# Kernel tuning notes

Hardware: AMD Instinct MI355X
Metric: run time of the kernel (lower is better)

Reference implementation:

```python
import jax, jax.numpy as jnp
import numpy as np

B, S, I, H, O = 64, 4096, 256, 256, 128


def setup_inputs() -> dict:
    key = jax.random.key(0)
    ks = jax.random.split(key, 7)
    s_in = 1.0 / np.sqrt(I)
    s_h = 1.0 / np.sqrt(H)
    return {
        "x": jax.random.normal(ks[0], (B, S, I), dtype=jnp.float32),
        "Wax_w": jax.random.uniform(ks[1], (H, I), jnp.float32, -s_in, s_in),
        "Wax_b": jax.random.uniform(ks[2], (H,), jnp.float32, -s_in, s_in),
        "Waa_w": jax.random.uniform(ks[3], (H, H), jnp.float32, -s_h, s_h),
        "Waa_b": jax.random.uniform(ks[4], (H,), jnp.float32, -s_h, s_h),
        "Wya_w": jax.random.uniform(ks[5], (O, H), jnp.float32, -s_h, s_h),
        "Wya_b": jax.random.uniform(ks[6], (O,), jnp.float32, -s_h, s_h),
    }


def reference(x, Wax_w, Wax_b, Waa_w, Waa_b, Wya_w, Wya_b):
    # Precompute input projections for all timesteps in one big GEMM: [B,S,H]
    xp = jnp.einsum("bsi,hi->bsh", x, Wax_w) + Wax_b

    def step(a_prev, xp_t):
        a_next = jnp.tanh(xp_t + a_prev @ Waa_w.T + Waa_b)
        return a_next, None

    a0 = jnp.zeros((x.shape[0], Waa_w.shape[0]), dtype=x.dtype)
    a_last, _ = jax.lax.scan(step, a0, jnp.swapaxes(xp, 0, 1))  # scan over S
    return jax.nn.sigmoid(a_last @ Wya_w.T + Wya_b)
```

## Files before the change

kernel.cpp:

```cpp
#include <hip/hip_runtime.h>
#include <hip/hip_fp16.h>


typedef _Float16 f16x8 __attribute__((ext_vector_type(8)));
typedef _Float16 f16x4 __attribute__((ext_vector_type(4)));
typedef _Float16 f16x2 __attribute__((ext_vector_type(2)));
typedef float    f32x4 __attribute__((ext_vector_type(4)));

#define FDOT2(a, b, c) __builtin_amdgcn_fdot2((a), (b), (c), false)

template <int D>
__device__ __forceinline__ float rorf(float v) {
    return __builtin_bit_cast(float,
        __builtin_amdgcn_update_dpp(0, __builtin_bit_cast(int, v),
                                    0x120 + D, 0xF, 0xF, true));
}

__global__ __launch_bounds__(512) void k_xp(
    const float* __restrict__ x, const float* __restrict__ Ww,
    const float* __restrict__ Wb, _Float16* __restrict__ xp,
    int c, int T_C, int logT)
{
    __shared__ __align__(16) _Float16 As[64 * 264];
    const int tid  = threadIdx.x;
    const int lane = tid & 63;
    const int wv   = tid >> 6;
    const int l15  = lane & 15;
    const int lk   = lane >> 4;
    const int n0   = wv * 32;

    f16x8 bfr[2][8];
#pragma unroll
    for (int nt = 0; nt < 2; ++nt) {
        const float* wrow = Ww + (size_t)(n0 + nt * 16 + l15) * 256;
#pragma unroll
        for (int kt = 0; kt < 8; ++kt) {
            const float4* wp = (const float4*)(wrow + kt * 32 + lk * 8);
            float4 v0 = wp[0], v1 = wp[1];
            f16x8 f;
            f[0] = (_Float16)v0.x; f[1] = (_Float16)v0.y;
            f[2] = (_Float16)v0.z; f[3] = (_Float16)v0.w;
            f[4] = (_Float16)v1.x; f[5] = (_Float16)v1.y;
            f[6] = (_Float16)v1.z; f[7] = (_Float16)v1.w;
            bfr[nt][kt] = f;
        }
    }
    const float bias0 = Wb[n0 + l15];
    const float bias1 = Wb[n0 + 16 + l15];

    {
        const int arow = tid >> 3;
        const int acol = (tid & 7) * 32;
        const int r    = blockIdx.x * 64 + arow;
        const int bb   = r >> logT;
        const int tl   = r & (T_C - 1);
        const float4* s4 = (const float4*)(x + ((size_t)(bb * 4096 + c * T_C + tl) << 8) + acol);
        _Float16* d = As + arow * 264 + acol;
#pragma unroll
        for (int q = 0; q < 4; ++q) {
            float4 v0 = s4[2 * q], v1 = s4[2 * q + 1];
            f16x8 p;
            p[0] = (_Float16)v0.x; p[1] = (_Float16)v0.y;
            p[2] = (_Float16)v0.z; p[3] = (_Float16)v0.w;
            p[4] = (_Float16)v1.x; p[5] = (_Float16)v1.y;
            p[6] = (_Float16)v1.z; p[7] = (_Float16)v1.w;
            *(f16x8*)(d + q * 8) = p;
        }
    }
    __syncthreads();

    f32x4 acc[4][2] = {};
#pragma unroll
    for (int kt = 0; kt < 8; ++kt) {
#pragma unroll
        for (int mt = 0; mt < 4; ++mt) {
            f16x8 af = *(const f16x8*)(As + (mt * 16 + l15) * 264 + kt * 32 + lk * 8);
            acc[mt][0] = __builtin_amdgcn_mfma_f32_16x16x32_f16(af, bfr[0][kt], acc[mt][0], 0, 0, 0);
            acc[mt][1] = __builtin_amdgcn_mfma_f32_16x16x32_f16(af, bfr[1][kt], acc[mt][1], 0, 0, 0);
        }
    }

    const int base = blockIdx.x * 64;
#pragma unroll
    for (int mt = 0; mt < 4; ++mt) {
        const int rr  = base + mt * 16 + lk * 4;
        const int bb2 = rr >> logT;
        const int tt  = rr & (T_C - 1);
#pragma unroll
        for (int nt = 0; nt < 2; ++nt) {
            const int   h    = n0 + nt * 16 + l15;
            const float bias = (nt == 0) ? bias0 : bias1;
            f16x4 pk;
#pragma unroll
            for (int r2 = 0; r2 < 4; ++r2) pk[r2] = (_Float16)(acc[mt][nt][r2] + bias);
            *(f16x4*)(xp + ((size_t)(bb2 * 256 + h)) * T_C + tt) = pk;
        }
    }
}

__global__ __launch_bounds__(1024) void k_rnn(
    const _Float16* __restrict__ xp, const float* __restrict__ Waa,
    const float* __restrict__ Wab, const float* __restrict__ Wya,
    const float* __restrict__ Wyb, float* __restrict__ out,
    unsigned short* __restrict__ a_state,
    int c, int T_C, int is_last)
{
    __shared__ __align__(16) _Float16 aL[2][16][24];
    __shared__ float afin[256];
    const int tid   = threadIdx.x;
    const int lane  = tid & 63;
    const int w     = tid >> 6;
    const int k     = lane & 15;
    const int g     = lane >> 4;
    const int rbase = w * 16 + g * 4;
    const int myrow = rbase + (k & 3);
    const int b     = blockIdx.x;
    const bool wlane = (k & 12) == 0;

    f16x2 wr[4][8];
#pragma unroll
    for (int i = 0; i < 4; ++i) {
        const float4* wp = (const float4*)(Waa + (size_t)(rbase + ((k + i) & 3)) * 256 + k * 16);
#pragma unroll
        for (int q = 0; q < 4; ++q) {
            float4 v = wp[q];
            f16x2 t0; t0[0] = (_Float16)v.x; t0[1] = (_Float16)v.y;
            f16x2 t1; t1[0] = (_Float16)v.z; t1[1] = (_Float16)v.w;
            wr[i][2 * q]     = t0;
            wr[i][2 * q + 1] = t1;
        }
    }
    const float bias = Wab[myrow];

    if (tid < 256) {
        unsigned short v = 0;
        if (c != 0) v = a_state[b * 256 + tid];
        aL[0][tid >> 4][tid & 15] = __builtin_bit_cast(_Float16, v);
    }
    __syncthreads();

    const _Float16* xph = xp + ((size_t)(b * 256 + myrow)) * T_C;
    f16x8 xq = *(const f16x8*)(xph);

    const _Float16* rp0 = &aL[0][k][0];
    const _Float16* rp1 = &aL[1][k][0];
    _Float16* wq0 = &aL[1][w][g * 4 + k];
    _Float16* wq1 = &aL[0][w][g * 4 + k];

#define RNN_STEP(J, FIN)                                                     \
    {                                                                        \
        const _Float16* rp = ((J) & 1) ? rp1 : rp0;                          \
        uint4 r0 = *(const uint4*)(rp);                                      \
        uint4 r1 = *(const uint4*)(rp + 8);                                  \
        float bx = bias + (float)xq[(J)];                                    \
        f16x2 a2[8];                                                         \
        a2[0] = __builtin_bit_cast(f16x2, r0.x);                             \
        a2[1] = __builtin_bit_cast(f16x2, r0.y);                             \
        a2[2] = __builtin_bit_cast(f16x2, r0.z);                             \
        a2[3] = __builtin_bit_cast(f16x2, r0.w);                             \
        a2[4] = __builtin_bit_cast(f16x2, r1.x);                             \
        a2[5] = __builtin_bit_cast(f16x2, r1.y);                             \
        a2[6] = __builtin_bit_cast(f16x2, r1.z);                             \
        a2[7] = __builtin_bit_cast(f16x2, r1.w);                             \
        float s0 = 0.f, s1 = 0.f, s2 = 0.f, s3 = 0.f;                        \
        _Pragma("unroll")                                                    \
        for (int q = 0; q < 8; ++q) {                                        \
            s0 = FDOT2(wr[0][q], a2[q], s0);                                 \
            s1 = FDOT2(wr[1][q], a2[q], s1);                                 \
            s2 = FDOT2(wr[2][q], a2[q], s2);                                 \
            s3 = FDOT2(wr[3][q], a2[q], s3);                                 \
        }                                                                    \
        float p0 = s0 + rorf<8>(s0);                                         \
        float p1 = s1 + rorf<8>(s1);                                         \
        float p2 = s2 + rorf<8>(s2);                                         \
        float p3 = s3 + rorf<8>(s3);                                         \
        float q0 = p0 + rorf<4>(p0);                                         \
        float q1 = p1 + rorf<4>(p1);                                         \
        float q2 = p2 + rorf<4>(p2);                                         \
        float q3 = p3 + rorf<4>(p3);                                         \
        float acc = (q0 + rorf<1>(q1)) + (rorf<2>(q2) + rorf<3>(q3));        \
        float z  = bx + acc;                                                 \
        float e2 = __expf(2.f * z);                                          \
        float a  = fmaf(-2.f, __builtin_amdgcn_rcpf(e2 + 1.f), 1.f);         \
        _Float16 ah = (_Float16)a;                                           \
        if (wlane) *(((J) & 1) ? wq1 : wq0) = ah;                            \
        if (FIN) {                                                           \
            afin[myrow] = a;                                                 \
            a_state[b * 256 + myrow] = __builtin_bit_cast(unsigned short, ah);\
        }                                                                    \
        asm volatile("s_waitcnt lgkmcnt(0)" ::: "memory");                   \
        __builtin_amdgcn_s_barrier();                                        \
        asm volatile("" ::: "memory");                                       \
    }

    for (int tb = 0; tb + 8 < T_C; tb += 8) {
        f16x8 xn = *(const f16x8*)(xph + tb + 8);
        RNN_STEP(0, false) RNN_STEP(1, false) RNN_STEP(2, false) RNN_STEP(3, false)
        RNN_STEP(4, false) RNN_STEP(5, false) RNN_STEP(6, false) RNN_STEP(7, false)
        xq = xn;
    }
    RNN_STEP(0, false) RNN_STEP(1, false) RNN_STEP(2, false) RNN_STEP(3, false)
    RNN_STEP(4, false) RNN_STEP(5, false) RNN_STEP(6, false) RNN_STEP(7, true)
#undef RNN_STEP

    if (is_last) {
        const int o  = tid >> 3;
        const int k8 = tid & 7;
        const float4* wp = (const float4*)(Wya + (size_t)o * 256 + k8 * 32);
        const float4* ap = (const float4*)(afin + k8 * 32);
        float s = 0.f;
#pragma unroll
        for (int i = 0; i < 8; ++i) {
            float4 wv4 = wp[i];
            float4 a4  = ap[i];
            s += wv4.x * a4.x + wv4.y * a4.y + wv4.z * a4.z + wv4.w * a4.w;
        }
        s += __shfl_xor(s, 1);
        s += __shfl_xor(s, 2);
        s += __shfl_xor(s, 4);
        if (k8 == 0)
            out[b * 128 + o] = __builtin_amdgcn_rcpf(1.f + __expf(-(s + Wyb[o])));
    }
}

extern "C" void kernel_launch(void* const* d_in, const int* in_sizes, int n_in,
                              void* d_out, int out_size, void* d_ws, size_t ws_size,
                              hipStream_t stream)
{
    (void)in_sizes; (void)n_in; (void)out_size;
    const float* x    = (const float*)d_in[0];
    const float* Waxw = (const float*)d_in[1];
    const float* Waxb = (const float*)d_in[2];
    const float* Waaw = (const float*)d_in[3];
    const float* Waab = (const float*)d_in[4];
    const float* Wyaw = (const float*)d_in[5];
    const float* Wyab = (const float*)d_in[6];
    float* out = (float*)d_out;

    int T_C = 4096, logT = 12;
    while (T_C > 32 && (size_t)64 * T_C * 256 * 2 + 32768 > ws_size) { T_C >>= 1; --logT; }

    _Float16* xp = (_Float16*)d_ws;
    unsigned short* a_state =
        (unsigned short*)((char*)d_ws + (size_t)64 * T_C * 256 * 2);

    const int nc = 4096 / T_C;
    for (int ci = 0; ci < nc; ++ci) {
        k_xp<<<dim3(T_C), dim3(512), 0, stream>>>(x, Waxw, Waxb, xp, ci, T_C, logT);
        k_rnn<<<dim3(64), dim3(1024), 0, stream>>>(xp, Waaw, Waab, Wyaw, Wyab,
                                                   out, a_state, ci, T_C, ci == nc - 1);
    }
}
```

Measured before the change: 2.271 ms.

## Batch 16 RNN chains per block and compute recurrence with MFMA

The recurrent kernel now processes 16 batch chains per block (4 blocks of 512 threads) and computes the hidden-state matvec as a 16x16x32 f16 MFMA GEMM, with the weights held in registers and the state double-buffered in LDS. This replaces 64 blocks doing per-chain fdot2 plus DPP reductions. The recurrent bias is folded into the input projection kernel, and xp loads are double-buffered across 4-step groups. The cost is that only 4 CUs do the serial recurrence, so each step's MFMA chain plus barrier latency sets the speed.

Measured after the change: 4.406 ms. 94.0% more time.

```diff
diff --git a/kernel.cpp b/kernel.cpp
--- a/kernel.cpp
+++ b/kernel.cpp
@@ -4,22 +4,12 @@
 
 typedef _Float16 f16x8 __attribute__((ext_vector_type(8)));
 typedef _Float16 f16x4 __attribute__((ext_vector_type(4)));
-typedef _Float16 f16x2 __attribute__((ext_vector_type(2)));
 typedef float    f32x4 __attribute__((ext_vector_type(4)));
-
-#define FDOT2(a, b, c) __builtin_amdgcn_fdot2((a), (b), (c), false)
-
-template <int D>
-__device__ __forceinline__ float rorf(float v) {
-    return __builtin_bit_cast(float,
-        __builtin_amdgcn_update_dpp(0, __builtin_bit_cast(int, v),
-                                    0x120 + D, 0xF, 0xF, true));
-}
 
 __global__ __launch_bounds__(512) void k_xp(
     const float* __restrict__ x, const float* __restrict__ Ww,
-    const float* __restrict__ Wb, _Float16* __restrict__ xp,
-    int c, int T_C, int logT)
+    const float* __restrict__ Wb, const float* __restrict__ Wab,
+    _Float16* __restrict__ xp, int c, int T_C, int logT)
 {
     __shared__ __align__(16) _Float16 As[64 * 264];
     const int tid  = threadIdx.x;
@@ -45,8 +35,8 @@
             bfr[nt][kt] = f;
         }
     }
-    const float bias0 = Wb[n0 + l15];
-    const float bias1 = Wb[n0 + 16 + l15];
+    const float bias0 = Wb[n0 + l15]      + Wab[n0 + l15];
+    const float bias1 = Wb[n0 + 16 + l15] + Wab[n0 + 16 + l15];
 
     {
         const int arow = tid >> 3;
@@ -98,128 +88,141 @@
     }
 }
 
-__global__ __launch_bounds__(1024) void k_rnn(
+__global__ __launch_bounds__(512)
+__attribute__((amdgpu_waves_per_eu(2, 2)))
+void k_rnn(
     const _Float16* __restrict__ xp, const float* __restrict__ Waa,
-    const float* __restrict__ Wab, const float* __restrict__ Wya,
-    const float* __restrict__ Wyb, float* __restrict__ out,
-    unsigned short* __restrict__ a_state,
+    const float* __restrict__ Wya, const float* __restrict__ Wyb,
+    float* __restrict__ out, unsigned short* __restrict__ a_state,
     int c, int T_C, int is_last)
 {
-    __shared__ __align__(16) _Float16 aL[2][16][24];
-    __shared__ float afin[256];
-    const int tid   = threadIdx.x;
-    const int lane  = tid & 63;
-    const int w     = tid >> 6;
-    const int k     = lane & 15;
-    const int g     = lane >> 4;
-    const int rbase = w * 16 + g * 4;
-    const int myrow = rbase + (k & 3);
-    const int b     = blockIdx.x;
-    const bool wlane = (k & 12) == 0;
-
-    f16x2 wr[4][8];
-#pragma unroll
-    for (int i = 0; i < 4; ++i) {
-        const float4* wp = (const float4*)(Waa + (size_t)(rbase + ((k + i) & 3)) * 256 + k * 16);
-#pragma unroll
-        for (int q = 0; q < 4; ++q) {
-            float4 v = wp[q];
-            f16x2 t0; t0[0] = (_Float16)v.x; t0[1] = (_Float16)v.y;
-            f16x2 t1; t1[0] = (_Float16)v.z; t1[1] = (_Float16)v.w;
-            wr[i][2 * q]     = t0;
-            wr[i][2 * q + 1] = t1;
-        }
-    }
-    const float bias = Wab[myrow];
-
-    if (tid < 256) {
-        unsigned short v = 0;
-        if (c != 0) v = a_state[b * 256 + tid];
-        aL[0][tid >> 4][tid & 15] = __builtin_bit_cast(_Float16, v);
+    __shared__ __align__(16) _Float16 aL[2][16][264];
+    const int tid  = threadIdx.x;
+    const int lane = tid & 63;
+    const int wv   = tid >> 6;
+    const int i15  = lane & 15;
+    const int g    = lane >> 4;
+    const int blk  = blockIdx.x;
+    const int chain_g = blk * 16 + i15;
+
+    f16x8 wa0[8], wa1[8];
+    {
+        const float* w0 = Waa + (size_t)(wv * 32 + i15) * 256 + g * 8;
+        const float* w1 = w0 + 16 * 256;
+#pragma unroll
+        for (int kk = 0; kk < 8; ++kk) {
+            const float4* p0 = (const float4*)(w0 + kk * 32);
+            float4 va = p0[0], vb = p0[1];
+            f16x8 f;
+            f[0] = (_Float16)va.x; f[1] = (_Float16)va.y;
+            f[2] = (_Float16)va.z; f[3] = (_Float16)va.w;
+            f[4] = (_Float16)vb.x; f[5] = (_Float16)vb.y;
+            f[6] = (_Float16)vb.z; f[7] = (_Float16)vb.w;
+            wa0[kk] = f;
+            const float4* p1 = (const float4*)(w1 + kk * 32);
+            float4 vc = p1[0], vd = p1[1];
+            f16x8 f2;
+            f2[0] = (_Float16)vc.x; f2[1] = (_Float16)vc.y;
+            f2[2] = (_Float16)vc.z; f2[3] = (_Float16)vc.w;
+            f2[4] = (_Float16)vd.x; f2[5] = (_Float16)vd.y;
+            f2[6] = (_Float16)vd.z; f2[7] = (_Float16)vd.w;
+            wa1[kk] = f2;
+        }
+    }
+
+    {
+        const int e = tid * 8, ch = e >> 8, k0 = e & 255;
+        if (c == 0) {
+            f16x8 z = {};
+            *(f16x8*)&aL[0][ch][k0] = z;
+        } else {
+            *(uint4*)&aL[0][ch][k0] =
+                *(const uint4*)&a_state[((size_t)(blk * 16 + ch) << 8) + k0];
+        }
     }
     __syncthreads();
 
-    const _Float16* xph = xp + ((size_t)(b * 256 + myrow)) * T_C;
-    f16x8 xq = *(const f16x8*)(xph);
-
-    const _Float16* rp0 = &aL[0][k][0];
-    const _Float16* rp1 = &aL[1][k][0];
-    _Float16* wq0 = &aL[1][w][g * 4 + k];
-    _Float16* wq1 = &aL[0][w][g * 4 + k];
-
-#define RNN_STEP(J, FIN)                                                     \
+    const _Float16* xpb =
+        xp + ((size_t)(chain_g * 256 + wv * 32 + g * 4)) * T_C;
+    f16x4 xqA[2][4], xqB[2][4];
+
+#define LOADX(X, T)                                                          \
     {                                                                        \
-        const _Float16* rp = ((J) & 1) ? rp1 : rp0;                          \
-        uint4 r0 = *(const uint4*)(rp);                                      \
-        uint4 r1 = *(const uint4*)(rp + 8);                                  \
-        float bx = bias + (float)xq[(J)];                                    \
-        f16x2 a2[8];                                                         \
-        a2[0] = __builtin_bit_cast(f16x2, r0.x);                             \
-        a2[1] = __builtin_bit_cast(f16x2, r0.y);                             \
-        a2[2] = __builtin_bit_cast(f16x2, r0.z);                             \
-        a2[3] = __builtin_bit_cast(f16x2, r0.w);                             \
-        a2[4] = __builtin_bit_cast(f16x2, r1.x);                             \
-        a2[5] = __builtin_bit_cast(f16x2, r1.y);                             \
-        a2[6] = __builtin_bit_cast(f16x2, r1.z);                             \
-        a2[7] = __builtin_bit_cast(f16x2, r1.w);                             \
-        float s0 = 0.f, s1 = 0.f, s2 = 0.f, s3 = 0.f;                        \
         _Pragma("unroll")                                                    \
-        for (int q = 0; q < 8; ++q) {                                        \
-            s0 = FDOT2(wr[0][q], a2[q], s0);                                 \
-            s1 = FDOT2(wr[1][q], a2[q], s1);                                 \
-            s2 = FDOT2(wr[2][q], a2[q], s2);                                 \
-            s3 = FDOT2(wr[3][q], a2[q], s3);                                 \
+        for (int t8 = 0; t8 < 2; ++t8) {                                     \
+            _Pragma("unroll")                                                \
+            for (int r = 0; r < 4; ++r)                                      \
+                X[t8][r] = *(const f16x4*)(xpb + (size_t)(t8 * 16 + r) * T_C + (T)); \
         }                                                                    \
-        float p0 = s0 + rorf<8>(s0);                                         \
-        float p1 = s1 + rorf<8>(s1);                                         \
-        float p2 = s2 + rorf<8>(s2);                                         \
-        float p3 = s3 + rorf<8>(s3);                                         \
-        float q0 = p0 + rorf<4>(p0);                                         \
-        float q1 = p1 + rorf<4>(p1);                                         \
-        float q2 = p2 + rorf<4>(p2);                                         \
-        float q3 = p3 + rorf<4>(p3);                                         \
-        float acc = (q0 + rorf<1>(q1)) + (rorf<2>(q2) + rorf<3>(q3));        \
-        float z  = bx + acc;                                                 \
-        float e2 = __expf(2.f * z);                                          \
-        float a  = fmaf(-2.f, __builtin_amdgcn_rcpf(e2 + 1.f), 1.f);         \
-        _Float16 ah = (_Float16)a;                                           \
-        if (wlane) *(((J) & 1) ? wq1 : wq0) = ah;                            \
-        if (FIN) {                                                           \
-            afin[myrow] = a;                                                 \
-            a_state[b * 256 + myrow] = __builtin_bit_cast(unsigned short, ah);\
+    }
+
+#define STEP(P, X, J)                                                        \
+    {                                                                        \
+        const _Float16* arow_ = &aL[(P)][i15][g * 8];                        \
+        f32x4 c0 = {0.f, 0.f, 0.f, 0.f}, c1 = {0.f, 0.f, 0.f, 0.f};          \
+        _Pragma("unroll")                                                    \
+        for (int kk = 0; kk < 8; ++kk) {                                     \
+            f16x8 bf = *(const f16x8*)(arow_ + kk * 32);                     \
+            c0 = __builtin_amdgcn_mfma_f32_16x16x32_f16(wa0[kk], bf, c0, 0, 0, 0); \
+            c1 = __builtin_amdgcn_mfma_f32_16x16x32_f16(wa1[kk], bf, c1, 0, 0, 0); \
         }                                                                    \
+        f16x4 o0, o1;                                                        \
+        _Pragma("unroll")                                                    \
+        for (int r = 0; r < 4; ++r) {                                        \
+            float z0 = c0[r] + (float)X[0][r][(J)];                          \
+            float e0 = __expf(2.f * z0);                                     \
+            o0[r] = (_Float16)fmaf(-2.f, __builtin_amdgcn_rcpf(e0 + 1.f), 1.f); \
+            float z1 = c1[r] + (float)X[1][r][(J)];                          \
+            float e1 = __expf(2.f * z1);                                     \
+            o1[r] = (_Float16)fmaf(-2.f, __builtin_amdgcn_rcpf(e1 + 1.f), 1.f); \
+        }                                                                    \
+        *(f16x4*)&aL[(P) ^ 1][i15][wv * 32 + g * 4]      = o0;               \
+        *(f16x4*)&aL[(P) ^ 1][i15][wv * 32 + 16 + g * 4] = o1;               \
         asm volatile("s_waitcnt lgkmcnt(0)" ::: "memory");                   \
         __builtin_amdgcn_s_barrier();                                        \
         asm volatile("" ::: "memory");                                       \
     }
 
-    for (int tb = 0; tb + 8 < T_C; tb += 8) {
-        f16x8 xn = *(const f16x8*)(xph + tb + 8);
-        RNN_STEP(0, false) RNN_STEP(1, false) RNN_STEP(2, false) RNN_STEP(3, false)
-        RNN_STEP(4, false) RNN_STEP(5, false) RNN_STEP(6, false) RNN_STEP(7, false)
-        xq = xn;
-    }
-    RNN_STEP(0, false) RNN_STEP(1, false) RNN_STEP(2, false) RNN_STEP(3, false)
-    RNN_STEP(4, false) RNN_STEP(5, false) RNN_STEP(6, false) RNN_STEP(7, true)
-#undef RNN_STEP
+    LOADX(xqA, 0)
+    for (int tb = 0; tb < T_C; tb += 8) {
+        LOADX(xqB, tb + 4)
+        STEP(0, xqA, 0) STEP(1, xqA, 1) STEP(0, xqA, 2) STEP(1, xqA, 3)
+        if (tb + 8 < T_C) LOADX(xqA, tb + 8)
+        STEP(0, xqB, 0) STEP(1, xqB, 1) STEP(0, xqB, 2) STEP(1, xqB, 3)
+    }
+#undef STEP
+#undef LOADX
+
+    {
+        const int e = tid * 8, ch = e >> 8, k0 = e & 255;
+        *(uint4*)&a_state[((size_t)(blk * 16 + ch) << 8) + k0] =
+            *(const uint4*)&aL[0][ch][k0];
+    }
 
     if (is_last) {
-        const int o  = tid >> 3;
-        const int k8 = tid & 7;
-        const float4* wp = (const float4*)(Wya + (size_t)o * 256 + k8 * 32);
-        const float4* ap = (const float4*)(afin + k8 * 32);
-        float s = 0.f;
-#pragma unroll
-        for (int i = 0; i < 8; ++i) {
-            float4 wv4 = wp[i];
-            float4 a4  = ap[i];
-            s += wv4.x * a4.x + wv4.y * a4.y + wv4.z * a4.z + wv4.w * a4.w;
-        }
-        s += __shfl_xor(s, 1);
-        s += __shfl_xor(s, 2);
-        s += __shfl_xor(s, 4);
-        if (k8 == 0)
-            out[b * 128 + o] = __builtin_amdgcn_rcpf(1.f + __expf(-(s + Wyb[o])));
+        const int ch = tid >> 5;
+        const int og = (tid & 31) * 4;
+        float s0 = Wyb[og], s1 = Wyb[og + 1], s2 = Wyb[og + 2], s3 = Wyb[og + 3];
+        for (int kk = 0; kk < 32; ++kk) {
+            f16x8 af = *(const f16x8*)&aL[0][ch][kk * 8];
+            float a[8];
+#pragma unroll
+            for (int j = 0; j < 8; ++j) a[j] = (float)af[j];
+#pragma unroll
+            for (int q = 0; q < 4; ++q) {
+                const float4* wp = (const float4*)(Wya + (size_t)(og + q) * 256 + kk * 8);
+                float4 w0 = wp[0], w1 = wp[1];
+                float t = w0.x * a[0] + w0.y * a[1] + w0.z * a[2] + w0.w * a[3]
+                        + w1.x * a[4] + w1.y * a[5] + w1.z * a[6] + w1.w * a[7];
+                if (q == 0) s0 += t; else if (q == 1) s1 += t;
+                else if (q == 2) s2 += t; else s3 += t;
+            }
+        }
+        float* op = out + (size_t)(blk * 16 + ch) * 128 + og;
+        op[0] = __builtin_amdgcn_rcpf(1.f + __expf(-s0));
+        op[1] = __builtin_amdgcn_rcpf(1.f + __expf(-s1));
+        op[2] = __builtin_amdgcn_rcpf(1.f + __expf(-s2));
+        op[3] = __builtin_amdgcn_rcpf(1.f + __expf(-s3));
     }
 }
 
@@ -246,8 +249,8 @@
 
     const int nc = 4096 / T_C;
     for (int ci = 0; ci < nc; ++ci) {
-        k_xp<<<dim3(T_C), dim3(512), 0, stream>>>(x, Waxw, Waxb, xp, ci, T_C, logT);
-        k_rnn<<<dim3(64), dim3(1024), 0, stream>>>(xp, Waaw, Waab, Wyaw, Wyab,
-                                                   out, a_state, ci, T_C, ci == nc - 1);
+        k_xp<<<dim3(T_C), dim3(512), 0, stream>>>(x, Waxw, Waxb, Waab, xp, ci, T_C, logT);
+        k_rnn<<<dim3(4), dim3(512), 0, stream>>>(xp, Waaw, Wyaw, Wyab,
+                                                 out, a_state, ci, T_C, ci == nc - 1);
     }
 }
```
